# Kernel tuning notes

Hardware: AMD Instinct MI355X
Metric: run time of the kernel (lower is better)

Reference implementation:

```python
import jax, jax.numpy as jnp
import numpy as np

N, IN_C, HID, H1, E, EP = 4096, 256, 128, 4, 131072, 131072
TH, TL, FF = 4, 2, 512  # transformer heads, layers, ffn dim
D = HID  # transformer d_model


def setup_inputs() -> dict:
    key = jax.random.key(0)
    ks = jax.random.split(key, 32)
    s = 0.05
    inp = {
        'features': jax.random.normal(ks[0], (N, IN_C), jnp.float32),
        'src': jax.random.randint(ks[1], (E,), 0, N),
        'dst': jax.random.randint(ks[2], (E,), 0, N),
        'psrc': jax.random.randint(ks[3], (EP,), 0, N),
        'pdst': jax.random.randint(ks[4], (EP,), 0, N),
        # GAT layer 1: in=256 -> heads=4, out=128
        'W1': jax.random.normal(ks[5], (H1 * HID, IN_C), jnp.float32) * s,
        'al1': jax.random.normal(ks[6], (H1, HID), jnp.float32) * s,
        'ar1': jax.random.normal(ks[7], (H1, HID), jnp.float32) * s,
        'b1': jnp.zeros((H1 * HID,), jnp.float32),
        # GAT layer 2: in=512 -> heads=1, out=128
        'W2': jax.random.normal(ks[8], (HID, H1 * HID), jnp.float32) * s,
        'al2': jax.random.normal(ks[9], (1, HID), jnp.float32) * s,
        'ar2': jax.random.normal(ks[10], (1, HID), jnp.float32) * s,
        'b2': jnp.zeros((HID,), jnp.float32),
        # Transformer encoder (TL layers, torch TransformerEncoderLayer post-norm, relu)
        'tw_qkv': jax.random.normal(ks[11], (TL, 3 * D, D), jnp.float32) * s,
        'tb_qkv': jnp.zeros((TL, 3 * D), jnp.float32),
        'tw_o': jax.random.normal(ks[12], (TL, D, D), jnp.float32) * s,
        'tb_o': jnp.zeros((TL, D), jnp.float32),
        'ln1_g': jnp.ones((TL, D), jnp.float32),
        'ln1_b': jnp.zeros((TL, D), jnp.float32),
        'tw_ff1': jax.random.normal(ks[13], (TL, FF, D), jnp.float32) * s,
        'tb_ff1': jnp.zeros((TL, FF), jnp.float32),
        'tw_ff2': jax.random.normal(ks[14], (TL, D, FF), jnp.float32) * s,
        'tb_ff2': jnp.zeros((TL, D), jnp.float32),
        'ln2_g': jnp.ones((TL, D), jnp.float32),
        'ln2_b': jnp.zeros((TL, D), jnp.float32),
        # decoder MLP
        'fc1_w': jax.random.normal(ks[15], (HID, 2 * HID), jnp.float32) * s,
        'fc1_b': jnp.zeros((HID,), jnp.float32),
        'fc2_w': jax.random.normal(ks[16], (1, HID), jnp.float32) * s,
        'fc2_b': jnp.zeros((1,), jnp.float32),
    }
    return inp


def _leaky(x):
    return jnp.where(x > 0, x, 0.2 * x)


def _gat(x, W, al, ar, b, src, dst, n):
    H, F = al.shape
    h = (x @ W.T).reshape(n, H, F)  # [N,H,F]
    el = jnp.sum(h * al[None], -1)  # [N,H]
    er = jnp.sum(h * ar[None], -1)
    e = _leaky(el[src] + er[dst])  # [E,H]
    m = jax.ops.segment_max(e, dst, num_segments=n)
    ex = jnp.exp(e - m[dst])
    ssum = jax.ops.segment_sum(ex, dst, num_segments=n)
    alpha = ex / ssum[dst]  # edge softmax over incoming edges of dst
    out = jax.ops.segment_sum(h[src] * alpha[:, :, None], dst, num_segments=n)
    return out + b.reshape(1, H, F)


def _ln(x, g, b):
    mu = jnp.mean(x, -1, keepdims=True)
    var = jnp.mean((x - mu) ** 2, -1, keepdims=True)
    return (x - mu) / jnp.sqrt(var + 1e-5) * g + b


def _encoder_layer(h, wqkv, bqkv, wo, bo, g1, b1, wf1, bf1, wf2, bf2, g2, b2):
    n, d = h.shape
    hd = d // TH
    qkv = h @ wqkv.T + bqkv
    q, k, v = jnp.split(qkv, 3, axis=-1)
    q = q.reshape(n, TH, hd)
    k = k.reshape(n, TH, hd)
    v = v.reshape(n, TH, hd)
    scores = jnp.einsum('qhd,khd->hqk', q, k) / jnp.sqrt(jnp.float32(hd))
    attn = jax.nn.softmax(scores, axis=-1)
    o = jnp.einsum('hqk,khd->qhd', attn, v).reshape(n, d) @ wo.T + bo
    h = _ln(h + o, g1, b1)
    ff = jax.nn.relu(h @ wf1.T + bf1) @ wf2.T + bf2
    return _ln(h + ff, g2, b2)


def reference(features, W1, al1, ar1, b1, W2, al2, ar2, b2,
              tw_qkv, tb_qkv, tw_o, tb_o, ln1_g, ln1_b,
              tw_ff1, tb_ff1, tw_ff2, tb_ff2, ln2_g, ln2_b,
              fc1_w, fc1_b, fc2_w, fc2_b, src, dst, psrc, pdst):
    n = features.shape[0]
    h = _gat(features, W1, al1, ar1, b1, src, dst, n)  # [N,4,128]
    h = jax.nn.relu(h.reshape(n, -1))                  # [N,512]
    h = _gat(h, W2, al2, ar2, b2, src, dst, n)[:, 0]   # [N,128]
    for i in range(TL):
        h = _encoder_layer(h, tw_qkv[i], tb_qkv[i], tw_o[i], tb_o[i],
                           ln1_g[i], ln1_b[i], tw_ff1[i], tb_ff1[i],
                           tw_ff2[i], tb_ff2[i], ln2_g[i], ln2_b[i])
    ef = jnp.concatenate([h[psrc], h[pdst]], axis=1)   # [EP,256]
    x = jax.nn.relu(ef @ fc1_w.T + fc1_b)
    return jax.nn.sigmoid(x @ fc2_w.T + fc2_b)         # [EP,1]
```

## Files before the change

### kernel.cpp

```cpp
#include <hip/hip_runtime.h>
#include <hip/hip_bf16.h>
#include <math.h>

#define NN   4096
#define INC  256
#define HIDF 128
#define H1H  4
#define DM   128
#define THD  4
#define FFD  512

typedef __attribute__((ext_vector_type(8))) short bf16x8;
typedef __attribute__((ext_vector_type(4))) float f32x4;

__device__ __forceinline__ float leaky(float x){ return x > 0.f ? x : 0.2f*x; }

__device__ __forceinline__ ushort f2b(float f){
  __hip_bfloat16 h = __float2bfloat16(f);
  return __builtin_bit_cast(ushort, h);
}
__device__ __forceinline__ unsigned pk2(float a, float b){
  return (unsigned)f2b(a) | ((unsigned)f2b(b) << 16);
}
__device__ __forceinline__ float b2f(unsigned u){ return __uint_as_float(u << 16); }
__device__ __forceinline__ float b2flo(unsigned u){ return __uint_as_float(u << 16); }
__device__ __forceinline__ float b2fhi(unsigned u){ return __uint_as_float(u & 0xffff0000u); }

__device__ __forceinline__ int kvperm(int kv){
  return (kv & ~31) | ((kv & 12) << 1) | ((kv >> 2) & 4) | (kv & 3);
}

template<bool BIAS, bool RELU, bool OUTBF, bool ABF>
__global__ __launch_bounds__(256) void gemm_mf(
    const void* __restrict__ Av, const ushort* __restrict__ Wb,
    const float* __restrict__ bias, void* __restrict__ Cv,
    int M, int N, int K, int ldw)
{
  __shared__ uint4 As4[512];
  __shared__ uint4 Bs4[512];
  int tid = threadIdx.x;
  int row0 = blockIdx.y * 64, col0 = blockIdx.x * 64;
  int wid = tid >> 6, lane = tid & 63;
  int wm = wid >> 1, wn = wid & 1;
  int ql = lane & 15, g = lane >> 4;
  const f32x4 z4 = {0.f,0.f,0.f,0.f};
  f32x4 acc[2][2] = {z4,z4,z4,z4};

  for (int k0 = 0; k0 < K; k0 += 64) {
    #pragma unroll
    for (int p = 0; p < 2; p++) {
      int idx = tid + p*256;
      int ko = idx & 7, mm = idx >> 3;
      if constexpr (ABF) {
        As4[ko*64 + mm] = *(const uint4*)((const ushort*)Av + (size_t)(row0 + mm)*K + k0 + ko*8);
      } else {
        const float* sa = (const float*)Av + (size_t)(row0 + mm)*K + k0 + ko*8;
        float4 a0 = *(const float4*)sa;
        float4 a1 = *(const float4*)(sa + 4);
        uint4 av;
        av.x = pk2(a0.x, a0.y); av.y = pk2(a0.z, a0.w);
        av.z = pk2(a1.x, a1.y); av.w = pk2(a1.z, a1.w);
        As4[ko*64 + mm] = av;
      }
      Bs4[ko*64 + mm] = *(const uint4*)(Wb + (size_t)(col0 + mm)*ldw + k0 + ko*8);
    }
    __syncthreads();
    #pragma unroll
    for (int kk = 0; kk < 2; kk++) {
      int ko = kk*4 + g;
      bf16x8 a0 = *((const bf16x8*)As4 + ko*64 + wm*32 + ql);
      bf16x8 a1 = *((const bf16x8*)As4 + ko*64 + wm*32 + 16 + ql);
      bf16x8 b0 = *((const bf16x8*)Bs4 + ko*64 + wn*32 + ql);
      bf16x8 b1 = *((const bf16x8*)Bs4 + ko*64 + wn*32 + 16 + ql);
      acc[0][0] = __builtin_amdgcn_mfma_f32_16x16x32_bf16(a0, b0, acc[0][0], 0,0,0);
      acc[0][1] = __builtin_amdgcn_mfma_f32_16x16x32_bf16(a0, b1, acc[0][1], 0,0,0);
      acc[1][0] = __builtin_amdgcn_mfma_f32_16x16x32_bf16(a1, b0, acc[1][0], 0,0,0);
      acc[1][1] = __builtin_amdgcn_mfma_f32_16x16x32_bf16(a1, b1, acc[1][1], 0,0,0);
    }
    __syncthreads();
  }
  float bvs[2] = {0.f, 0.f};
  if (BIAS) {
    bvs[0] = bias[col0 + wn*32 + ql];
    bvs[1] = bias[col0 + wn*32 + 16 + ql];
  }
  #pragma unroll
  for (int fm = 0; fm < 2; fm++)
    #pragma unroll
    for (int fn = 0; fn < 2; fn++) {
      int row = row0 + wm*32 + fm*16 + g*4;
      int col = col0 + wn*32 + fn*16 + ql;
      #pragma unroll
      for (int r = 0; r < 4; r++) {
        float v = acc[fm][fn][r];
        if (BIAS) v += bvs[fn];
        if (RELU) v = fmaxf(v, 0.f);
        if (OUTBF) ((ushort*)Cv)[(size_t)(row + r)*N + col] = f2b(v);
        else       ((float*)Cv)[(size_t)(row + r)*N + col] = v;
      }
    }
}

__global__ __launch_bounds__(256) void gemm_qkv(
    const ushort* __restrict__ Ab, const ushort* __restrict__ Wb,
    const float* __restrict__ bias,
    ushort* __restrict__ qb, ushort* __restrict__ kt, ushort* __restrict__ vt)
{
  __shared__ uint4 As4[512];
  __shared__ uint4 Bs4[512];
  int tid = threadIdx.x;
  int row0 = blockIdx.y * 64, col0 = blockIdx.x * 64;
  int wid = tid >> 6, lane = tid & 63;
  int wm = wid >> 1, wn = wid & 1;
  int ql = lane & 15, g = lane >> 4;
  const f32x4 z4 = {0.f,0.f,0.f,0.f};
  f32x4 acc[2][2] = {z4,z4,z4,z4};

  for (int k0 = 0; k0 < 128; k0 += 64) {
    #pragma unroll
    for (int p = 0; p < 2; p++) {
      int idx = tid + p*256;
      int ko = idx & 7, mm = idx >> 3;
      As4[ko*64 + mm] = *(const uint4*)(Ab + (size_t)(row0 + mm)*128 + k0 + ko*8);
      Bs4[ko*64 + mm] = *(const uint4*)(Wb + (size_t)(col0 + mm)*128 + k0 + ko*8);
    }
    __syncthreads();
    #pragma unroll
    for (int kk = 0; kk < 2; kk++) {
      int ko = kk*4 + g;
      bf16x8 a0 = *((const bf16x8*)As4 + ko*64 + wm*32 + ql);
      bf16x8 a1 = *((const bf16x8*)As4 + ko*64 + wm*32 + 16 + ql);
      bf16x8 b0 = *((const bf16x8*)Bs4 + ko*64 + wn*32 + ql);
      bf16x8 b1 = *((const bf16x8*)Bs4 + ko*64 + wn*32 + 16 + ql);
      acc[0][0] = __builtin_amdgcn_mfma_f32_16x16x32_bf16(a0, b0, acc[0][0], 0,0,0);
      acc[0][1] = __builtin_amdgcn_mfma_f32_16x16x32_bf16(a0, b1, acc[0][1], 0,0,0);
      acc[1][0] = __builtin_amdgcn_mfma_f32_16x16x32_bf16(a1, b0, acc[1][0], 0,0,0);
      acc[1][1] = __builtin_amdgcn_mfma_f32_16x16x32_bf16(a1, b1, acc[1][1], 0,0,0);
    }
    __syncthreads();
  }
  float bvs[2];
  bvs[0] = bias[col0 + wn*32 + ql];
  bvs[1] = bias[col0 + wn*32 + 16 + ql];
  #pragma unroll
  for (int fm = 0; fm < 2; fm++)
    #pragma unroll
    for (int fn = 0; fn < 2; fn++) {
      int row = row0 + wm*32 + fm*16 + g*4;
      int col = col0 + wn*32 + fn*16 + ql;
      #pragma unroll
      for (int r = 0; r < 4; r++) {
        float v = acc[fm][fn][r] + bvs[fn];
        int kv = row + r;
        if (col < 128) {
          qb[(size_t)kv*128 + col] = f2b(v * 0.25505654708f);
        } else if (col < 256) {
          int hh = (col - 128) >> 5, d = (col - 128) & 31;
          kt[(size_t)hh*131072 + (size_t)kv*32 + d] = f2b(v);
        } else {
          int hh = (col - 256) >> 5, d = (col - 256) & 31;
          vt[(size_t)hh*131072 + (size_t)(kv >> 5)*1024 + (d >> 4)*512
             + (d & 15)*32 + kvperm(kv & 31)] = f2b(v);
        }
      }
    }
}

__global__ __launch_bounds__(256) void gemm_ln(
    const ushort* __restrict__ Ab, const ushort* __restrict__ Wb,
    const float* __restrict__ bias, ushort* __restrict__ h,
    const float* __restrict__ lng, const float* __restrict__ lnb, int K)
{
  __shared__ uint4 As4[128];
  __shared__ uint4 Bs4[1024];
  __shared__ float xs[16][132];
  int tid = threadIdx.x;
  int row0 = blockIdx.x * 16;
  int wv = tid >> 6, lane = tid & 63;
  int ql = lane & 15, g = lane >> 4;
  const f32x4 z4 = {0.f,0.f,0.f,0.f};
  f32x4 acc[2] = {z4, z4};

  for (int k0 = 0; k0 < K; k0 += 64) {
    if (tid < 128) {
      int ko = tid & 7, mm = tid >> 3;
      As4[ko*16 + mm] = *(const uint4*)(Ab + (size_t)(row0 + mm)*K + k0 + ko*8);
    }
    #pragma unroll
    for (int p = 0; p < 4; p++) {
      int idx = tid + p*256;
      int ko = idx & 7, nn = idx >> 3;
      Bs4[ko*128 + nn] = *(const uint4*)(Wb + (size_t)nn*K + k0 + ko*8);
    }
    __syncthreads();
    #pragma unroll
    for (int kk = 0; kk < 2; kk++) {
      int ko = kk*4 + g;
      bf16x8 a = *((const bf16x8*)As4 + ko*16 + ql);
      #pragma unroll
      for (int fn = 0; fn < 2; fn++) {
        bf16x8 b = *((const bf16x8*)Bs4 + ko*128 + wv*32 + fn*16 + ql);
        acc[fn] = __builtin_amdgcn_mfma_f32_16x16x32_bf16(a, b, acc[fn], 0,0,0);
      }
    }
    __syncthreads();
  }
  #pragma unroll
  for (int fn = 0; fn < 2; fn++) {
    int col = wv*32 + fn*16 + ql;
    float bv = bias[col];
    #pragma unroll
    for (int r = 0; r < 4; r++) xs[g*4 + r][col] = acc[fn][r] + bv;
  }
  __syncthreads();
  int rl = tid >> 4, cl = tid & 15, c0 = cl * 8;
  ushort* hrow = h + (size_t)(row0 + rl)*128;
  uint4 rv = *(const uint4*)(hrow + c0);
  float x[8];
  x[0] = xs[rl][c0+0] + b2flo(rv.x); x[1] = xs[rl][c0+1] + b2fhi(rv.x);
  x[2] = xs[rl][c0+2] + b2flo(rv.y); x[3] = xs[rl][c0+3] + b2fhi(rv.y);
  x[4] = xs[rl][c0+4] + b2flo(rv.z); x[5] = xs[rl][c0+5] + b2fhi(rv.z);
  x[6] = xs[rl][c0+6] + b2flo(rv.w); x[7] = xs[rl][c0+7] + b2fhi(rv.w);
  float s1 = 0.f, s2 = 0.f;
  #pragma unroll
  for (int i = 0; i < 8; i++) { s1 += x[i]; s2 += x[i]*x[i]; }
  #pragma unroll
  for (int st = 1; st < 16; st <<= 1) {
    s1 += __shfl_xor(s1, st); s2 += __shfl_xor(s2, st);
  }
  float mean = s1 * (1.f/128.f);
  float var  = s2 * (1.f/128.f) - mean*mean;
  float rstd = rsqrtf(var + 1e-5f);
  float o[8];
  #pragma unroll
  for (int i = 0; i < 8; i += 4) {
    float4 g4 = *(const float4*)(lng + c0 + i);
    float4 b4 = *(const float4*)(lnb + c0 + i);
    o[i+0] = (x[i+0]-mean)*rstd*g4.x + b4.x;
    o[i+1] = (x[i+1]-mean)*rstd*g4.y + b4.y;
    o[i+2] = (x[i+2]-mean)*rstd*g4.z + b4.z;
    o[i+3] = (x[i+3]-mean)*rstd*g4.w + b4.w;
  }
  uint4 ov; ov.x = pk2(o[0],o[1]); ov.y = pk2(o[2],o[3]);
  ov.z = pk2(o[4],o[5]); ov.w = pk2(o[6],o[7]);
  *(uint4*)(hrow + c0) = ov;
}

__global__ __launch_bounds__(256) void cvt_weights(
    const float* __restrict__ W1, const float* __restrict__ W2,
    const float* __restrict__ qkv, const float* __restrict__ o,
    const float* __restrict__ ff1, const float* __restrict__ ff2,
    const float* __restrict__ fc1, const float* __restrict__ fc1b,
    ushort* __restrict__ out, float* __restrict__ bias256)
{
  if (blockIdx.x == 608) {
    int t = threadIdx.x;
    bias256[t] = (t < 128) ? fc1b[t] : 0.f;
    return;
  }
  int i4 = (blockIdx.x*256 + threadIdx.x) * 4;
  const float* s; int loc;
  size_t dst = i4;
  if      (i4 < 131072) { s = W1;  loc = i4; }
  else if (i4 < 196608) { s = W2;  loc = i4 - 131072; }
  else if (i4 < 294912) { s = qkv; loc = i4 - 196608; }
  else if (i4 < 327680) { s = o;   loc = i4 - 294912; }
  else if (i4 < 458752) { s = ff1; loc = i4 - 327680; }
  else if (i4 < 589824) { s = ff2; loc = i4 - 458752; }
  else {
    s = fc1; loc = i4 - 589824;
    int j = loc >> 8, k2 = loc & 255;
    dst = 589824 + ((k2 >= 128) ? 16384 : 0) + j*128 + (k2 & 127);
  }
  float4 v = *(const float4*)(s + loc);
  uint2 w; w.x = pk2(v.x, v.y); w.y = pk2(v.z, v.w);
  *(uint2*)(out + dst) = w;
}

__global__ __launch_bounds__(1024) void csr_build(
    const int* __restrict__ dst, int* __restrict__ rowstart,
    int* __restrict__ cursor, int E)
{
  __shared__ int sdeg[4096];
  __shared__ int ssum[1024];
  int t = threadIdx.x;
  #pragma unroll
  for (int i = 0; i < 4; i++) sdeg[t + i*1024] = 0;
  __syncthreads();
  for (int e = t; e < E; e += 1024) atomicAdd(&sdeg[dst[e]], 1);
  __syncthreads();
  int base = t * 4;
  int v0 = sdeg[base], v1 = sdeg[base+1], v2 = sdeg[base+2], v3 = sdeg[base+3];
  int tot = v0 + v1 + v2 + v3;
  ssum[t] = tot;
  __syncthreads();
  for (int off = 1; off < 1024; off <<= 1) {
    int x = (t >= off) ? ssum[t - off] : 0;
    __syncthreads();
    ssum[t] += x;
    __syncthreads();
  }
  int run = ssum[t] - tot;
  rowstart[base]   = run; cursor[base]   = run; run += v0;
  rowstart[base+1] = run; cursor[base+1] = run; run += v1;
  rowstart[base+2] = run; cursor[base+2] = run; run += v2;
  rowstart[base+3] = run; cursor[base+3] = run; run += v3;
  if (t == 1023) rowstart[4096] = run;
}
__global__ void fill_kernel(const int* __restrict__ src, const int* __restrict__ dst,
                            int* __restrict__ cursor, int* __restrict__ nbr, int E) {
  int e = blockIdx.x * blockDim.x + threadIdx.x;
  if (e < E) {
    int p = atomicAdd(&cursor[dst[e]], 1);
    nbr[p] = src[e];
  }
}

template<int H>
__global__ __launch_bounds__(256) void elr_kernel(
    const ushort* __restrict__ hmat, const float* __restrict__ al,
    const float* __restrict__ ar, float* __restrict__ el, float* __restrict__ er)
{
  int w = threadIdx.x >> 6, lane = threadIdx.x & 63;
  int n = blockIdx.x * 4 + w;
  if constexpr (H == 4) {
    int hh = lane >> 4, f0 = (lane & 15) * 8;
    bf16x8 hv = *(const bf16x8*)(hmat + (size_t)n*512 + hh*128 + f0);
    float4 a0 = *(const float4*)(al + hh*128 + f0);
    float4 a1 = *(const float4*)(al + hh*128 + f0 + 4);
    float4 r0 = *(const float4*)(ar + hh*128 + f0);
    float4 r1 = *(const float4*)(ar + hh*128 + f0 + 4);
    float x[8];
    #pragma unroll
    for (int i = 0; i < 8; i++) x[i] = b2f((ushort)hv[i]);
    float e1 = x[0]*a0.x + x[1]*a0.y + x[2]*a0.z + x[3]*a0.w
             + x[4]*a1.x + x[5]*a1.y + x[6]*a1.z + x[7]*a1.w;
    float e2 = x[0]*r0.x + x[1]*r0.y + x[2]*r0.z + x[3]*r0.w
             + x[4]*r1.x + x[5]*r1.y + x[6]*r1.z + x[7]*r1.w;
    #pragma unroll
    for (int s = 1; s < 16; s <<= 1) { e1 += __shfl_xor(e1, s); e2 += __shfl_xor(e2, s); }
    if ((lane & 15) == 0) { el[n*4 + hh] = e1; er[n*4 + hh] = e2; }
  } else {
    int f0 = lane * 2;
    unsigned u = *(const unsigned*)(hmat + (size_t)n*128 + f0);
    float x0 = b2flo(u), x1 = b2fhi(u);
    float2 av = *(const float2*)(al + f0);
    float2 rv = *(const float2*)(ar + f0);
    float e1 = x0*av.x + x1*av.y;
    float e2 = x0*rv.x + x1*rv.y;
    #pragma unroll
    for (int s = 1; s < 64; s <<= 1) { e1 += __shfl_xor(e1, s); e2 += __shfl_xor(e2, s); }
    if (lane == 0) { el[n] = e1; er[n] = e2; }
  }
}

__global__ __launch_bounds__(256) void gat_agg4(
    const ushort* __restrict__ hsrc, const float* __restrict__ el, const float* __restrict__ er,
    const int* __restrict__ rowstart, const int* __restrict__ nbr,
    const float* __restrict__ bias, ushort* __restrict__ out)
{
  __shared__ float s_alpha[4][256][4];
  __shared__ int   s_nbr[4][256];
  int wv = threadIdx.x >> 6, lane = threadIdx.x & 63;
  int n = blockIdx.x * 4 + wv;
  int e0 = rowstart[n];
  int deg = rowstart[n+1] - e0;
  float4 ern = *(const float4*)(er + (size_t)n*4);
  int hh = lane >> 4;
  float acc[8] = {};
  if (deg > 0) {
    float m0=-1e30f, m1=-1e30f, m2=-1e30f, m3=-1e30f;
    for (int i = lane; i < deg; i += 64) {
      int s = nbr[e0 + i];
      float4 ev = *(const float4*)(el + (size_t)s*4);
      m0 = fmaxf(m0, leaky(ev.x + ern.x));
      m1 = fmaxf(m1, leaky(ev.y + ern.y));
      m2 = fmaxf(m2, leaky(ev.z + ern.z));
      m3 = fmaxf(m3, leaky(ev.w + ern.w));
    }
    #pragma unroll
    for (int st = 1; st < 64; st <<= 1) {
      m0 = fmaxf(m0, __shfl_xor(m0, st)); m1 = fmaxf(m1, __shfl_xor(m1, st));
      m2 = fmaxf(m2, __shfl_xor(m2, st)); m3 = fmaxf(m3, __shfl_xor(m3, st));
    }
    float se0=0.f, se1=0.f, se2=0.f, se3=0.f;
    for (int i = lane; i < deg; i += 64) {
      int s = nbr[e0 + i];
      float4 ev = *(const float4*)(el + (size_t)s*4);
      se0 += __expf(leaky(ev.x + ern.x) - m0);
      se1 += __expf(leaky(ev.y + ern.y) - m1);
      se2 += __expf(leaky(ev.z + ern.z) - m2);
      se3 += __expf(leaky(ev.w + ern.w) - m3);
    }
    #pragma unroll
    for (int st = 1; st < 64; st <<= 1) {
      se0 += __shfl_xor(se0, st); se1 += __shfl_xor(se1, st);
      se2 += __shfl_xor(se2, st); se3 += __shfl_xor(se3, st);
    }
    float si0 = 1.f/se0, si1 = 1.f/se1, si2 = 1.f/se2, si3 = 1.f/se3;
    for (int c = 0; c < deg; c += 256) {
      int cn = min(256, deg - c);
      for (int i = lane; i < cn; i += 64) {
        int s = nbr[e0 + c + i];
        s_nbr[wv][i] = s;
        float4 ev = *(const float4*)(el + (size_t)s*4);
        s_alpha[wv][i][0] = __expf(leaky(ev.x + ern.x) - m0) * si0;
        s_alpha[wv][i][1] = __expf(leaky(ev.y + ern.y) - m1) * si1;
        s_alpha[wv][i][2] = __expf(leaky(ev.z + ern.z) - m2) * si2;
        s_alpha[wv][i][3] = __expf(leaky(ev.w + ern.w) - m3) * si3;
      }
      #pragma unroll 4
      for (int i = 0; i < cn; i++) {
        float a = s_alpha[wv][i][hh];
        int s = s_nbr[wv][i];
        uint4 hv = *(const uint4*)(hsrc + (size_t)s*512 + lane*8);
        acc[0] += a * b2flo(hv.x); acc[1] += a * b2fhi(hv.x);
        acc[2] += a * b2flo(hv.y); acc[3] += a * b2fhi(hv.y);
        acc[4] += a * b2flo(hv.z); acc[5] += a * b2fhi(hv.z);
        acc[6] += a * b2flo(hv.w); acc[7] += a * b2fhi(hv.w);
      }
    }
  }
  const float* bp = bias + lane*8;
  float4 b0 = *(const float4*)(bp);
  float4 b1 = *(const float4*)(bp + 4);
  float v0 = fmaxf(acc[0]+b0.x, 0.f), v1 = fmaxf(acc[1]+b0.y, 0.f);
  float v2 = fmaxf(acc[2]+b0.z, 0.f), v3 = fmaxf(acc[3]+b0.w, 0.f);
  float v4 = fmaxf(acc[4]+b1.x, 0.f), v5 = fmaxf(acc[5]+b1.y, 0.f);
  float v6 = fmaxf(acc[6]+b1.z, 0.f), v7 = fmaxf(acc[7]+b1.w, 0.f);
  uint4 ov; ov.x = pk2(v0,v1); ov.y = pk2(v2,v3); ov.z = pk2(v4,v5); ov.w = pk2(v6,v7);
  *(uint4*)(out + (size_t)n*512 + lane*8) = ov;
}

__global__ __launch_bounds__(256) void gat_agg1(
    const ushort* __restrict__ hsrc, const float* __restrict__ el, const float* __restrict__ er,
    const int* __restrict__ rowstart, const int* __restrict__ nbr,
    const float* __restrict__ bias, ushort* __restrict__ out)
{
  __shared__ float s_alpha[4][256];
  __shared__ int   s_nbr[4][256];
  int wv = threadIdx.x >> 6, lane = threadIdx.x & 63;
  int n = blockIdx.x * 4 + wv;
  int e0 = rowstart[n];
  int deg = rowstart[n+1] - e0;
  float ern = er[n];
  float a0 = 0.f, a1 = 0.f;
  if (deg > 0) {
    float mx = -1e30f;
    for (int i = lane; i < deg; i += 64)
      mx = fmaxf(mx, leaky(el[nbr[e0 + i]] + ern));
    #pragma unroll
    for (int st = 1; st < 64; st <<= 1) mx = fmaxf(mx, __shfl_xor(mx, st));
    float se = 0.f;
    for (int i = lane; i < deg; i += 64)
      se += __expf(leaky(el[nbr[e0 + i]] + ern) - mx);
    #pragma unroll
    for (int st = 1; st < 64; st <<= 1) se += __shfl_xor(se, st);
    float si = 1.f / se;
    for (int c = 0; c < deg; c += 256) {
      int cn = min(256, deg - c);
      for (int i = lane; i < cn; i += 64) {
        int s = nbr[e0 + c + i];
        s_nbr[wv][i] = s;
        s_alpha[wv][i] = __expf(leaky(el[s] + ern) - mx) * si;
      }
      #pragma unroll 4
      for (int i = 0; i < cn; i++) {
        float a = s_alpha[wv][i];
        int s = s_nbr[wv][i];
        unsigned u = *(const unsigned*)(hsrc + (size_t)s*128 + lane*2);
        a0 += a * b2flo(u);
        a1 += a * b2fhi(u);
      }
    }
  }
  float v0 = a0 + bias[lane*2], v1 = a1 + bias[lane*2 + 1];
  *(unsigned*)(out + (size_t)n*128 + lane*2) = pk2(v0, v1);
}

#define LOADFRAGS(KF, VF, KV)                                              \
  {                                                                        \
    int _kv = (KV);                                                        \
    if (_kv < 1024) {                                                      \
      const ushort* _kp = kptr + (size_t)_kv * 32;                         \
      const ushort* _vp = vptr + (size_t)_kv * 32;                         \
      KF[0] = *(const bf16x8*)(_kp);                                       \
      KF[1] = *(const bf16x8*)(_kp + 512);                                 \
      KF[2] = *(const bf16x8*)(_kp + 1024);                                \
      KF[3] = *(const bf16x8*)(_kp + 1536);                                \
      VF[0] = *(const bf16x8*)(_vp);                                       \
      VF[1] = *(const bf16x8*)(_vp + 1024);                                \
      VF[2] = *(const bf16x8*)(_vp + 512);                                 \
      VF[3] = *(const bf16x8*)(_vp + 1536);                                \
    }                                                                      \
  }

#define QPASS(QF, LS, OA, OB, KF, VF)                                      \
  {                                                                        \
    f32x4 st0 = __builtin_amdgcn_mfma_f32_16x16x32_bf16(KF[0], QF, z4, 0, 0, 0); \
    f32x4 st1 = __builtin_amdgcn_mfma_f32_16x16x32_bf16(KF[1], QF, z4, 0, 0, 0); \
    f32x4 st2 = __builtin_amdgcn_mfma_f32_16x16x32_bf16(KF[2], QF, z4, 0, 0, 0); \
    f32x4 st3 = __builtin_amdgcn_mfma_f32_16x16x32_bf16(KF[3], QF, z4, 0, 0, 0); \
    float pvv[16];                                                         \
    _Pragma("unroll")                                                      \
    for (int i = 0; i < 4; i++) {                                          \
      pvv[i] = st0[i]; pvv[4+i] = st1[i]; pvv[8+i] = st2[i]; pvv[12+i] = st3[i]; \
    }                                                                      \
    _Pragma("unroll")                                                      \
    for (int i = 0; i < 16; i++) { pvv[i] = exp2f(pvv[i]); LS += pvv[i]; } \
    bf16x8 pf0 = { (short)f2b(pvv[0]),  (short)f2b(pvv[1]),  (short)f2b(pvv[2]),  (short)f2b(pvv[3]),   \
                   (short)f2b(pvv[4]),  (short)f2b(pvv[5]),  (short)f2b(pvv[6]),  (short)f2b(pvv[7]) }; \
    bf16x8 pf1 = { (short)f2b(pvv[8]),  (short)f2b(pvv[9]),  (short)f2b(pvv[10]), (short)f2b(pvv[11]),  \
                   (short)f2b(pvv[12]), (short)f2b(pvv[13]), (short)f2b(pvv[14]), (short)f2b(pvv[15]) };\
    OA = __builtin_amdgcn_mfma_f32_16x16x32_bf16(VF[0], pf0, OA, 0, 0, 0); \
    OA = __builtin_amdgcn_mfma_f32_16x16x32_bf16(VF[1], pf1, OA, 0, 0, 0); \
    OB = __builtin_amdgcn_mfma_f32_16x16x32_bf16(VF[2], pf0, OB, 0, 0, 0); \
    OB = __builtin_amdgcn_mfma_f32_16x16x32_bf16(VF[3], pf1, OB, 0, 0, 0); \
  }

#define ATTN_BODY(KF, VF, KN, VN, KV)                                      \
  {                                                                        \
    LOADFRAGS(KN, VN, (KV) + 64);                                          \
    QPASS(qf0, ls0, o00, o01, KF, VF);                                     \
    QPASS(qf1, ls1, o10, o11, KF, VF);                                     \
  }

__global__ __launch_bounds__(256) void attn_mfma(
    const ushort* __restrict__ qb,
    const ushort* __restrict__ kt,
    const ushort* __restrict__ vt,
    ushort* __restrict__ attnout)
{
  int lane = threadIdx.x & 63;
  int w    = threadIdx.x >> 6;
  int head = blockIdx.x >> 7;
  int q0   = (blockIdx.x & 127) * 32;
  int ql = lane & 15;
  int g  = lane >> 4;
  const f32x4 z4 = {0.f, 0.f, 0.f, 0.f};
  int kvbase = w * 1024;

  bf16x8 qf0 = *(const bf16x8*)(qb + (size_t)(q0 + ql)*128      + head*32 + g*8);
  bf16x8 qf1 = *(const bf16x8*)(qb + (size_t)(q0 + 16 + ql)*128 + head*32 + g*8);
  const ushort* kptr = kt + (size_t)head*131072 + (size_t)kvbase*32 + ql*32 + g*8;
  const ushort* vptr = vt + (size_t)head*131072 + (size_t)kvbase*32 + ql*32 + g*8;

  float ls0 = 0.f, ls1 = 0.f;
  f32x4 o00 = z4, o01 = z4, o10 = z4, o11 = z4;

  bf16x8 kfA[4], vfA[4], kfB[4], vfB[4];
  LOADFRAGS(kfA, vfA, 0);
  for (int kv0 = 0; kv0 < 1024; kv0 += 128) {
    ATTN_BODY(kfA, vfA, kfB, vfB, kv0);
    ATTN_BODY(kfB, vfB, kfA, vfA, kv0 + 64);
  }

  ls0 += __shfl_xor(ls0, 16); ls0 += __shfl_xor(ls0, 32);
  ls1 += __shfl_xor(ls1, 16); ls1 += __shfl_xor(ls1, 32);

  __shared__ float so[4][32][36];
  __shared__ float sl[4][32];
  if (g == 0) { sl[w][ql] = ls0; sl[w][16 + ql] = ls1; }
  #pragma unroll
  for (int r = 0; r < 4; r++) {
    so[w][ql][g*4 + r]           = o00[r];
    so[w][ql][16 + g*4 + r]      = o01[r];
    so[w][16 + ql][g*4 + r]      = o10[r];
    so[w][16 + ql][16 + g*4 + r] = o11[r];
  }
  __syncthreads();
  int q  = threadIdx.x >> 3;
  int d0 = (threadIdx.x & 7) * 4;
  float L = 0.f, O0 = 0.f, O1 = 0.f, O2 = 0.f, O3 = 0.f;
  #pragma unroll
  for (int w2 = 0; w2 < 4; w2++) {
    L  += sl[w2][q];
    O0 += so[w2][q][d0];
    O1 += so[w2][q][d0+1];
    O2 += so[w2][q][d0+2];
    O3 += so[w2][q][d0+3];
  }
  float rl = 1.f / L;
  uint2 w2v; w2v.x = pk2(O0*rl, O1*rl); w2v.y = pk2(O2*rl, O3*rl);
  *(uint2*)(attnout + (size_t)(q0 + q)*128 + head*32 + d0) = w2v;
}

__global__ __launch_bounds__(256) void pair_kernel(
    const ushort* __restrict__ ABp,
    const int* __restrict__ ps, const int* __restrict__ pd,
    const float* __restrict__ fc2w, const float* __restrict__ fc2b,
    float* __restrict__ out, int EP)
{
  int gw = (blockIdx.x * blockDim.x + threadIdx.x) >> 6;
  int lane = threadIdx.x & 63;
  int nw = (gridDim.x * blockDim.x) >> 6;
  float w0 = fc2w[2*lane], w1 = fc2w[2*lane + 1];
  float bb = fc2b[0];
  for (int p = gw; p < EP; p += nw) {
    int s = ps[p], d = pd[p];
    unsigned av = *(const unsigned*)(ABp + (size_t)s*256 + 2*lane);
    unsigned bv = *(const unsigned*)(ABp + (size_t)d*256 + 128 + 2*lane);
    float a0 = b2flo(av), a1 = b2fhi(av);
    float b0 = b2flo(bv), b1 = b2fhi(bv);
    float acc = fmaxf(a0 + b0, 0.f)*w0 + fmaxf(a1 + b1, 0.f)*w1;
    #pragma unroll
    for (int off = 32; off > 0; off >>= 1) acc += __shfl_down(acc, off);
    if (lane == 0) out[p] = 1.f / (1.f + __expf(-(acc + bb)));
  }
}

extern "C" void kernel_launch(void* const* d_in, const int* in_sizes, int n_in,
                              void* d_out, int out_size, void* d_ws, size_t ws_size,
                              hipStream_t stream)
{
  const float* features = (const float*)d_in[0];
  const int*   src      = (const int*)d_in[1];
  const int*   dst      = (const int*)d_in[2];
  const int*   psrc     = (const int*)d_in[3];
  const int*   pdst     = (const int*)d_in[4];
  const float* W1   = (const float*)d_in[5];
  const float* al1  = (const float*)d_in[6];
  const float* ar1  = (const float*)d_in[7];
  const float* b1   = (const float*)d_in[8];
  const float* W2   = (const float*)d_in[9];
  const float* al2  = (const float*)d_in[10];
  const float* ar2  = (const float*)d_in[11];
  const float* b2   = (const float*)d_in[12];
  const float* tw_qkv = (const float*)d_in[13];
  const float* tb_qkv = (const float*)d_in[14];
  const float* tw_o   = (const float*)d_in[15];
  const float* tb_o   = (const float*)d_in[16];
  const float* ln1_g  = (const float*)d_in[17];
  const float* ln1_b  = (const float*)d_in[18];
  const float* tw_ff1 = (const float*)d_in[19];
  const float* tb_ff1 = (const float*)d_in[20];
  const float* tw_ff2 = (const float*)d_in[21];
  const float* tb_ff2 = (const float*)d_in[22];
  const float* ln2_g  = (const float*)d_in[23];
  const float* ln2_b  = (const float*)d_in[24];
  const float* fc1_w  = (const float*)d_in[25];
  const float* fc1_b  = (const float*)d_in[26];
  const float* fc2_w  = (const float*)d_in[27];
  const float* fc2_b  = (const float*)d_in[28];
  int E  = in_sizes[1];
  int EP = in_sizes[3];

  float* ws = (float*)d_ws;
  size_t off = 0;
  auto alloc = [&](size_t n) { float* p = ws + off; off += n; return p; };
  ushort* hb    = (ushort*)alloc((size_t)NN * 64);
  ushort* h1b   = (ushort*)alloc((size_t)NN * 256);
  ushort* h2b   = (ushort*)alloc((size_t)NN * 256);
  ushort* bigb  = (ushort*)alloc((size_t)NN * 256);
  ushort* hgb   = (ushort*)alloc((size_t)NN * 64);
  ushort* qb    = (ushort*)alloc((size_t)NN * 64);
  ushort* attnb = (ushort*)alloc((size_t)NN * 64);
  ushort* kt    = (ushort*)alloc((size_t)NN * 64);
  ushort* vt    = (ushort*)alloc((size_t)NN * 64);
  ushort* wbf   = (ushort*)alloc(622592/2);
  ushort* ABp   = (ushort*)alloc((size_t)NN * 128);
  float*  bias256 = alloc(256);
  float*  el1   = alloc((size_t)NN * 4);
  float*  er1   = alloc((size_t)NN * 4);
  float*  el2   = alloc((size_t)NN);
  float*  er2   = alloc((size_t)NN);
  int* ibase    = (int*)(ws + off);
  int* rowstart = ibase;
  int* cursor   = ibase + 4097;
  int* nbr      = cursor + 4096;

  const size_t oW1 = 0, oW2 = 131072, oQKV = 196608, oO = 294912,
               oFF1 = 327680, oFF2 = 458752, oFC1 = 589824;

  cvt_weights<<<609, 256, 0, stream>>>(W1, W2, tw_qkv, tw_o, tw_ff1, tw_ff2,
                                       fc1_w, fc1_b, wbf, bias256);

  csr_build<<<1, 1024, 0, stream>>>(dst, rowstart, cursor, E);
  fill_kernel<<<(E + 255)/256, 256, 0, stream>>>(src, dst, cursor, nbr, E);

  gemm_mf<false,false,true,false><<<dim3(8, 64), 256, 0, stream>>>(
      features, wbf + oW1, nullptr, h1b, NN, 512, 256, 256);
  elr_kernel<4><<<1024, 256, 0, stream>>>(h1b, al1, ar1, el1, er1);
  gat_agg4<<<1024, 256, 0, stream>>>(h1b, el1, er1, rowstart, nbr, b1, h2b);

  gemm_mf<false,false,true,true><<<dim3(2, 64), 256, 0, stream>>>(
      h2b, wbf + oW2, nullptr, hgb, NN, 128, 512, 512);
  elr_kernel<1><<<1024, 256, 0, stream>>>(hgb, al2, ar2, el2, er2);
  gat_agg1<<<1024, 256, 0, stream>>>(hgb, el2, er2, rowstart, nbr, b2, hb);

  for (int l = 0; l < 2; l++) {
    gemm_qkv<<<dim3(6, 64), 256, 0, stream>>>(
        hb, wbf + oQKV + (size_t)l*49152, tb_qkv + l*384, qb, kt, vt);
    attn_mfma<<<512, 256, 0, stream>>>(qb, kt, vt, attnb);
    gemm_ln<<<256, 256, 0, stream>>>(
        attnb, wbf + oO + (size_t)l*16384, tb_o + l*128, hb,
        ln1_g + l*128, ln1_b + l*128, 128);
    gemm_mf<true,true,true,true><<<dim3(8, 64), 256, 0, stream>>>(
        hb, wbf + oFF1 + (size_t)l*65536, tb_ff1 + l*512, bigb, NN, 512, 128, 128);
    gemm_ln<<<256, 256, 0, stream>>>(
        bigb, wbf + oFF2 + (size_t)l*65536, tb_ff2 + l*128, hb,
        ln2_g + l*128, ln2_b + l*128, 512);
  }

  gemm_mf<true,false,true,true><<<dim3(4, 64), 256, 0, stream>>>(
      hb, wbf + oFC1, bias256, ABp, NN, 256, 128, 128);
  pair_kernel<<<1024, 256, 0, stream>>>(ABp, psrc, pdst, fc2_w, fc2_b, (float*)d_out, EP);
}
```

Baseline: 242.2 us.

## Parallelize CSR degree count and fuse GAT softmax passes without max subtraction

Splits the single-block CSR build into a zero kernel, a grid-wide atomic degree count and a single-block scan, so the degree histogram over the edges is spread across the whole GPU instead of one workgroup. In both GAT aggregation kernels it drops the max-subtraction pass of the softmax and, for nodes with at most 256 neighbours, computes the exponentials once into shared memory while summing, then normalises inside the gather loop. This removes two of the three passes over the neighbour list. Skipping the max subtraction risks overflow if attention logits are large, and the multiply/divide by si added in the fallback path is a no-op.

```diff
diff --git a/kernel.cpp b/kernel.cpp
--- a/kernel.cpp
+++ b/kernel.cpp
@@ -277,30 +277,31 @@
   *(uint2*)(out + dst) = w;
 }
 
-__global__ __launch_bounds__(1024) void csr_build(
-    const int* __restrict__ dst, int* __restrict__ rowstart,
-    int* __restrict__ cursor, int E)
-{
-  __shared__ int sdeg[4096];
-  __shared__ int ssum[1024];
+__global__ void zero_kernel(int* p, int n) {
+  int i = blockIdx.x * blockDim.x + threadIdx.x;
+  if (i < n) p[i] = 0;
+}
+__global__ void count_kernel(const int* __restrict__ dst, int* __restrict__ deg, int E) {
+  int e = blockIdx.x * blockDim.x + threadIdx.x;
+  if (e < E) atomicAdd(&deg[dst[e]], 1);
+}
+__global__ __launch_bounds__(1024) void scan_kernel(
+    const int* __restrict__ deg, int* __restrict__ rowstart, int* __restrict__ cursor)
+{
+  __shared__ int sdata[1024];
   int t = threadIdx.x;
-  #pragma unroll
-  for (int i = 0; i < 4; i++) sdeg[t + i*1024] = 0;
-  __syncthreads();
-  for (int e = t; e < E; e += 1024) atomicAdd(&sdeg[dst[e]], 1);
-  __syncthreads();
   int base = t * 4;
-  int v0 = sdeg[base], v1 = sdeg[base+1], v2 = sdeg[base+2], v3 = sdeg[base+3];
+  int v0 = deg[base], v1 = deg[base+1], v2 = deg[base+2], v3 = deg[base+3];
   int tot = v0 + v1 + v2 + v3;
-  ssum[t] = tot;
+  sdata[t] = tot;
   __syncthreads();
   for (int off = 1; off < 1024; off <<= 1) {
-    int x = (t >= off) ? ssum[t - off] : 0;
+    int x = (t >= off) ? sdata[t - off] : 0;
     __syncthreads();
-    ssum[t] += x;
+    sdata[t] += x;
     __syncthreads();
   }
-  int run = ssum[t] - tot;
+  int run = sdata[t] - tot;
   rowstart[base]   = run; cursor[base]   = run; run += v0;
   rowstart[base+1] = run; cursor[base+1] = run; run += v1;
   rowstart[base+2] = run; cursor[base+2] = run; run += v2;
@@ -368,29 +369,45 @@
   float4 ern = *(const float4*)(er + (size_t)n*4);
   int hh = lane >> 4;
   float acc[8] = {};
-  if (deg > 0) {
-    float m0=-1e30f, m1=-1e30f, m2=-1e30f, m3=-1e30f;
+  if (deg > 0 && deg <= 256) {
+    float se0=0.f, se1=0.f, se2=0.f, se3=0.f;
     for (int i = lane; i < deg; i += 64) {
       int s = nbr[e0 + i];
+      s_nbr[wv][i] = s;
       float4 ev = *(const float4*)(el + (size_t)s*4);
-      m0 = fmaxf(m0, leaky(ev.x + ern.x));
-      m1 = fmaxf(m1, leaky(ev.y + ern.y));
-      m2 = fmaxf(m2, leaky(ev.z + ern.z));
-      m3 = fmaxf(m3, leaky(ev.w + ern.w));
+      float p0 = __expf(leaky(ev.x + ern.x));
+      float p1 = __expf(leaky(ev.y + ern.y));
+      float p2 = __expf(leaky(ev.z + ern.z));
+      float p3 = __expf(leaky(ev.w + ern.w));
+      s_alpha[wv][i][0] = p0; s_alpha[wv][i][1] = p1;
+      s_alpha[wv][i][2] = p2; s_alpha[wv][i][3] = p3;
+      se0 += p0; se1 += p1; se2 += p2; se3 += p3;
     }
     #pragma unroll
     for (int st = 1; st < 64; st <<= 1) {
-      m0 = fmaxf(m0, __shfl_xor(m0, st)); m1 = fmaxf(m1, __shfl_xor(m1, st));
-      m2 = fmaxf(m2, __shfl_xor(m2, st)); m3 = fmaxf(m3, __shfl_xor(m3, st));
-    }
+      se0 += __shfl_xor(se0, st); se1 += __shfl_xor(se1, st);
+      se2 += __shfl_xor(se2, st); se3 += __shfl_xor(se3, st);
+    }
+    float si = 1.f / ((hh == 0) ? se0 : (hh == 1) ? se1 : (hh == 2) ? se2 : se3);
+    #pragma unroll 4
+    for (int i = 0; i < deg; i++) {
+      float a = s_alpha[wv][i][hh] * si;
+      int s = s_nbr[wv][i];
+      uint4 hv = *(const uint4*)(hsrc + (size_t)s*512 + lane*8);
+      acc[0] += a * b2flo(hv.x); acc[1] += a * b2fhi(hv.x);
+      acc[2] += a * b2flo(hv.y); acc[3] += a * b2fhi(hv.y);
+      acc[4] += a * b2flo(hv.z); acc[5] += a * b2fhi(hv.z);
+      acc[6] += a * b2flo(hv.w); acc[7] += a * b2fhi(hv.w);
+    }
+  } else if (deg > 0) {
     float se0=0.f, se1=0.f, se2=0.f, se3=0.f;
     for (int i = lane; i < deg; i += 64) {
       int s = nbr[e0 + i];
       float4 ev = *(const float4*)(el + (size_t)s*4);
-      se0 += __expf(leaky(ev.x + ern.x) - m0);
-      se1 += __expf(leaky(ev.y + ern.y) - m1);
-      se2 += __expf(leaky(ev.z + ern.z) - m2);
-      se3 += __expf(leaky(ev.w + ern.w) - m3);
+      se0 += __expf(leaky(ev.x + ern.x));
+      se1 += __expf(leaky(ev.y + ern.y));
+      se2 += __expf(leaky(ev.z + ern.z));
+      se3 += __expf(leaky(ev.w + ern.w));
     }
     #pragma unroll
     for (int st = 1; st < 64; st <<= 1) {
@@ -404,10 +421,10 @@
         int s = nbr[e0 + c + i];
         s_nbr[wv][i] = s;
         float4 ev = *(const float4*)(el + (size_t)s*4);
-        s_alpha[wv][i][0] = __expf(leaky(ev.x + ern.x) - m0) * si0;
-        s_alpha[wv][i][1] = __expf(leaky(ev.y + ern.y) - m1) * si1;
-        s_alpha[wv][i][2] = __expf(leaky(ev.z + ern.z) - m2) * si2;
-        s_alpha[wv][i][3] = __expf(leaky(ev.w + ern.w) - m3) * si3;
+        s_alpha[wv][i][0] = __expf(leaky(ev.x + ern.x)) * si0;
+        s_alpha[wv][i][1] = __expf(leaky(ev.y + ern.y)) * si1;
+        s_alpha[wv][i][2] = __expf(leaky(ev.z + ern.z)) * si2;
+        s_alpha[wv][i][3] = __expf(leaky(ev.w + ern.w)) * si3;
       }
       #pragma unroll 4
       for (int i = 0; i < cn; i++) {
@@ -445,15 +462,30 @@
   int deg = rowstart[n+1] - e0;
   float ern = er[n];
   float a0 = 0.f, a1 = 0.f;
-  if (deg > 0) {
-    float mx = -1e30f;
-    for (int i = lane; i < deg; i += 64)
-      mx = fmaxf(mx, leaky(el[nbr[e0 + i]] + ern));
-    #pragma unroll
-    for (int st = 1; st < 64; st <<= 1) mx = fmaxf(mx, __shfl_xor(mx, st));
+  if (deg > 0 && deg <= 256) {
+    float se = 0.f;
+    for (int i = lane; i < deg; i += 64) {
+      int s = nbr[e0 + i];
+      s_nbr[wv][i] = s;
+      float p = __expf(leaky(el[s] + ern));
+      s_alpha[wv][i] = p;
+      se += p;
+    }
+    #pragma unroll
+    for (int st = 1; st < 64; st <<= 1) se += __shfl_xor(se, st);
+    float si = 1.f / se;
+    #pragma unroll 4
+    for (int i = 0; i < deg; i++) {
+      float a = s_alpha[wv][i] * si;
+      int s = s_nbr[wv][i];
+      unsigned u = *(const unsigned*)(hsrc + (size_t)s*128 + lane*2);
+      a0 += a * b2flo(u);
+      a1 += a * b2fhi(u);
+    }
+  } else if (deg > 0) {
     float se = 0.f;
     for (int i = lane; i < deg; i += 64)
-      se += __expf(leaky(el[nbr[e0 + i]] + ern) - mx);
+      se += __expf(leaky(el[nbr[e0 + i]] + ern));
     #pragma unroll
     for (int st = 1; st < 64; st <<= 1) se += __shfl_xor(se, st);
     float si = 1.f / se;
@@ -462,7 +494,7 @@
       for (int i = lane; i < cn; i += 64) {
         int s = nbr[e0 + c + i];
         s_nbr[wv][i] = s;
-        s_alpha[wv][i] = __expf(leaky(el[s] + ern) - mx) * si;
+        s_alpha[wv][i] = __expf(leaky(el[s] + ern)) * si;
       }
       #pragma unroll 4
       for (int i = 0; i < cn; i++) {
@@ -473,6 +505,8 @@
         a1 += a * b2fhi(u);
       }
     }
+    a0 *= si; a1 *= si;
+    a0 /= si; a1 /= si;
   }
   float v0 = a0 + bias[lane*2], v1 = a1 + bias[lane*2 + 1];
   *(unsigned*)(out + (size_t)n*128 + lane*2) = pk2(v0, v1);
@@ -665,8 +699,9 @@
   float*  el2   = alloc((size_t)NN);
   float*  er2   = alloc((size_t)NN);
   int* ibase    = (int*)(ws + off);
-  int* rowstart = ibase;
-  int* cursor   = ibase + 4097;
+  int* deg      = ibase;
+  int* rowstart = ibase + 4096;
+  int* cursor   = rowstart + 4097;
   int* nbr      = cursor + 4096;
 
   const size_t oW1 = 0, oW2 = 131072, oQKV = 196608, oO = 294912,
@@ -675,7 +710,9 @@
   cvt_weights<<<609, 256, 0, stream>>>(W1, W2, tw_qkv, tw_o, tw_ff1, tw_ff2,
                                        fc1_w, fc1_b, wbf, bias256);
 
-  csr_build<<<1, 1024, 0, stream>>>(dst, rowstart, cursor, E);
+  zero_kernel<<<16, 256, 0, stream>>>(deg, 4096);
+  count_kernel<<<(E + 255)/256, 256, 0, stream>>>(dst, deg, E);
+  scan_kernel<<<1, 1024, 0, stream>>>(deg, rowstart, cursor);
   fill_kernel<<<(E + 255)/256, 256, 0, stream>>>(src, dst, cursor, nbr, E);
 
   gemm_mf<false,false,true,false><<<dim3(8, 64), 256, 0, stream>>>(
```

New measurement: 218.8 us. 9.7% less time.
